# Kernel tuning notes

Hardware: AMD Instinct MI355X
Metric: run time of the kernel (lower is better)

The kernel has to match this reference:

```python
import jax, jax.numpy as jnp
import numpy as np

B, C, D, H, W, K = 2, 192, 48, 48, 48, 7
EPS_LN = 1e-6
EPS_GRN = 1e-6


def setup_inputs() -> dict:
    key = jax.random.key(0)
    ks = jax.random.split(key, 8)
    sc = 0.02
    return {
        "x": jax.random.normal(ks[0], (B, C, D, H, W), jnp.float32),
        # depthwise conv kernel in DHWIO layout: [K,K,K,1,C] (torch weight [C,1,K,K,K])
        "conv_w": jax.random.normal(ks[1], (K, K, K, 1, C), jnp.float32) * sc,
        "conv_b": jnp.zeros((C,), jnp.float32),
        "ln_g": jnp.ones((C,), jnp.float32),
        "ln_b": jnp.zeros((C,), jnp.float32),
        "w1": jax.random.normal(ks[2], (C, 4 * C), jnp.float32) * sc,
        "b1": jnp.zeros((4 * C,), jnp.float32),
        "grn_gamma": jax.random.normal(ks[3], (4 * C,), jnp.float32) * sc,
        "grn_beta": jax.random.normal(ks[4], (4 * C,), jnp.float32) * sc,
        "w2": jax.random.normal(ks[5], (4 * C, C), jnp.float32) * sc,
        "b2": jnp.zeros((C,), jnp.float32),
    }


def reference(x, conv_w, conv_b, ln_g, ln_b, w1, b1, grn_gamma, grn_beta, w2, b2):
    c = x.shape[1]
    # NCDHW -> NDHWC (channels-last, as Permute([0,2,3,4,1]) after the conv)
    xc = jnp.transpose(x, (0, 2, 3, 4, 1))
    # depthwise conv3d, kernel 7, pad 3 (SAME for stride 1)
    y = jax.lax.conv_general_dilated(
        xc, conv_w, window_strides=(1, 1, 1), padding="SAME",
        dimension_numbers=("NDHWC", "DHWIO", "NDHWC"),
        feature_group_count=c,
    ) + conv_b
    # LayerNorm over channel dim, eps=1e-6 (biased variance, like torch)
    mu = jnp.mean(y, axis=-1, keepdims=True)
    var = jnp.mean(jnp.square(y - mu), axis=-1, keepdims=True)
    y = (y - mu) * jax.lax.rsqrt(var + EPS_LN) * ln_g + ln_b
    # MLP up + exact GELU
    y = jax.nn.gelu(y @ w1 + b1, approximate=False)
    # GRN: global L2 over spatial dims per channel
    gx = jnp.sqrt(jnp.sum(y * y, axis=(1, 2, 3), keepdims=True))  # [B,1,1,1,4C]
    nx = gx / (jnp.mean(gx, axis=-1, keepdims=True) + EPS_GRN)
    y = grn_gamma * (y * nx) + grn_beta + y
    # MLP down, permute back, residual
    y = y @ w2 + b2
    return jnp.transpose(y, (0, 4, 1, 2, 3)) + x
```

## Files before the change

### kernel.cpp

```cpp
#include <hip/hip_runtime.h>
#include <math.h>

#define Bn 2
#define Cn 192
#define Dn 48
#define Hn 48
#define Wn 48
#define C4 768
#define DHW (Dn*Hn*Wn)
#define CDHW ((long)Cn*DHW)

typedef __attribute__((ext_vector_type(8))) short bf16x8;
typedef __attribute__((ext_vector_type(4))) float f32x4;

__device__ inline float bf2f(unsigned short u) {
    union { float f; unsigned int i; } v; v.i = ((unsigned int)u) << 16; return v.f;
}
__device__ inline unsigned short f2bf(float f) {
    union { float f; unsigned int i; } v; v.f = f;
    unsigned int r = v.i + 0x7FFFu + ((v.i >> 16) & 1u);
    return (unsigned short)(r >> 16);
}
__device__ inline float blo(unsigned int u) {
    union { unsigned int i; float f; } v; v.i = u << 16; return v.f;
}
__device__ inline float bhi(unsigned int u) {
    union { unsigned int i; float f; } v; v.i = u & 0xffff0000u; return v.f;
}
__device__ inline unsigned int cvtpk_bf16(float lo, float hi) {
    unsigned int r;
    asm("v_cvt_pk_bf16_f32 %0, %1, %2" : "=v"(r) : "v"(lo), "v"(hi));
    return r;
}
__device__ inline float gelu_tanh(float v) {
    float u = v * fmaf(0.0356774081f, v * v, 0.7978845608f);
    float a = fabsf(u);
    float t = __expf(-2.0f * a);
    float th = (1.0f - t) / (1.0f + t);
    th = copysignf(th, u);
    return 0.5f * v * (1.0f + th);
}

__global__ __launch_bounds__(256)
void xpad_k(const float* __restrict__ x, unsigned short* __restrict__ xbf)
{
    int u = blockIdx.x * 256 + threadIdx.x;
    int j = u & 7;
    int row = u >> 3;
    unsigned short* orow = xbf + ((size_t)row << 6);
    uint4 o = {0u, 0u, 0u, 0u};
    if (j >= 1 && j <= 6) {
        const float* xr = x + (size_t)row * 48 + (8 * j - 8);
        float4 a = *(const float4*)xr;
        float4 b = *(const float4*)(xr + 4);
        o.x = cvtpk_bf16(a.x, a.y); o.y = cvtpk_bf16(a.z, a.w);
        o.z = cvtpk_bf16(b.x, b.y); o.w = cvtpk_bf16(b.z, b.w);
    }
    *(uint4*)(orow + 8 * j) = o;
}

__global__ __launch_bounds__(256)
void btoep_k(const float* __restrict__ cw, unsigned short* __restrict__ btp)
{
    int idx = blockIdx.x * 256 + threadIdx.x;
    int lane = idx & 63;
    int t = idx >> 6;
    int kdkh = t % 49, c = t / 49;
    int n = lane & 15, g = lane >> 4;
    unsigned short v[8];
#pragma unroll
    for (int j = 0; j < 8; ++j) {
        int kw = 8 * g + j - n - 5;
        v[j] = (kw >= 0 && kw <= 6) ? f2bf(cw[(kdkh * 7 + kw) * Cn + c])
                                    : (unsigned short)0;
    }
    *(uint4*)(btp + (size_t)idx * 8) = *(uint4*)v;
}

#define CTD 16
#define CHD (CTD+6)
#define CHH 22

__global__ __launch_bounds__(128)
void conv_dw(const unsigned short* __restrict__ xbf, const unsigned short* __restrict__ btp,
             const float* __restrict__ cb, unsigned short* __restrict__ yc)
{
    __shared__ unsigned int xt[CHD * CHH * 16];
    int c = blockIdx.y;
    int s = blockIdx.x;
    int wt = s % 3, ht = (s / 3) % 3, dt = s / 9;
    int d0 = dt * 16, h0 = ht * 16, w0 = wt * 16;
    int tid = threadIdx.x;

    const unsigned short* xc = xbf + ((size_t)c * 2304 << 6);
    for (int u = tid; u < CHD * CHH * 4; u += 128) {
        int g = u & 3, r2 = u >> 2;
        int hh2 = r2 % CHH, dd = r2 / CHH;
        int gd = d0 - 3 + dd, gh = h0 - 3 + hh2;
        uint4 v = {0u, 0u, 0u, 0u};
        if ((unsigned)gd < 48u && (unsigned)gh < 48u)
            v = *(const uint4*)(xc + (((size_t)gd * 48 + gh) << 6) + w0 + 8 * g);
        *(uint4*)&xt[(r2 << 4) + ((g ^ (r2 & 3)) << 2)] = v;
    }
    __syncthreads();

    int lane = tid & 63, wv = tid >> 6;
    int lr = lane & 15, g = lane >> 4;
    float bias = cb[c];
    f32x4 acc[8];
#pragma unroll
    for (int t = 0; t < 8; ++t) acc[t] = (f32x4){bias, bias, bias, bias};

    const unsigned short* bchan = btp + (size_t)c * 49 * 512;
    const unsigned short* xt16 = (const unsigned short*)xt;

    for (int kh = 0; kh < 7; ++kh) {
        bf16x8 Bf[7];
#pragma unroll
        for (int kd = 0; kd < 7; ++kd)
            Bf[kd] = *(const bf16x8*)(bchan + (size_t)((kd * 7 + kh) * 64 + lane) * 8);
#pragma unroll
        for (int p = 0; p < 14; ++p) {
            int r2 = (8 * wv + p) * CHH + kh + lr;
            bf16x8 Af = *(const bf16x8*)(xt16 + (r2 << 5) + ((g ^ (r2 & 3)) << 3));
#pragma unroll
            for (int kd = 0; kd < 7; ++kd) {
                int t = p - kd;
                if (t < 0 || t > 7) continue;
                acc[t] = __builtin_amdgcn_mfma_f32_16x16x32_bf16(Af, Bf[kd], acc[t], 0, 0, 0);
            }
        }
    }

    unsigned short* yb = yc + (long)c * DHW;
#pragma unroll
    for (int t = 0; t < 8; ++t) {
        int d = d0 + 8 * wv + t;
#pragma unroll
        for (int i = 0; i < 4; ++i) {
            int h = h0 + g * 4 + i;
            yb[((long)d * 48 + h) * 48 + w0 + lr] = f2bf(acc[t][i]);
        }
    }
}

__global__ __launch_bounds__(256)
void ln_kernel(const unsigned short* __restrict__ yc, const float* __restrict__ g,
               const float* __restrict__ lb, unsigned short* __restrict__ y1)
{
    __shared__ float tile[Cn * Wn];
    __shared__ float qs1[4][48], qs2[4][48];
    __shared__ float mu_s[Wn], rs_s[Wn];
    int dh = blockIdx.x;
    long rowbase = (long)dh * Wn;
    for (int l = threadIdx.x; l < Cn * 24; l += 256) {
        int c = l / 24, wp = l % 24;
        unsigned int u = *(const unsigned int*)&yc[rowbase + (long)c * DHW + wp * 2];
        tile[c * Wn + wp * 2]     = blo(u);
        tile[c * Wn + wp * 2 + 1] = bhi(u);
    }
    __syncthreads();
    if (threadIdx.x < 192) {
        int w = threadIdx.x >> 2, q = threadIdx.x & 3;
        float s1 = 0.f, s2 = 0.f;
        for (int cc = 0; cc < 48; ++cc) {
            float v = tile[(cc * 4 + q) * Wn + w];
            s1 += v; s2 = fmaf(v, v, s2);
        }
        qs1[q][w] = s1; qs2[q][w] = s2;
    }
    __syncthreads();
    if (threadIdx.x < 48) {
        int w = threadIdx.x;
        float s1 = qs1[0][w] + qs1[1][w] + qs1[2][w] + qs1[3][w];
        float s2 = qs2[0][w] + qs2[1][w] + qs2[2][w] + qs2[3][w];
        float mu = s1 * (1.0f / Cn);
        float var = s2 * (1.0f / Cn) - mu * mu;
        mu_s[w] = mu;
        rs_s[w] = rsqrtf(var + 1e-6f);
    }
    __syncthreads();
    long obase = (long)dh * Wn * Cn;
    for (int l = threadIdx.x; l < Cn * Wn; l += 256) {
        int w = l / Cn, c = l % Cn;
        float val = (tile[c * Wn + w] - mu_s[w]) * rs_s[w] * g[c] + lb[c];
        y1[obase + l] = f2bf(val);
    }
}

__global__ __launch_bounds__(256)
void wtrans(const float* __restrict__ W, unsigned short* __restrict__ Wt, int K, int N)
{
    int idx = blockIdx.x * 256 + threadIdx.x;
    if (idx >= K * N) return;
    int n = idx / K, k = idx % K;
    Wt[idx] = f2bf(W[(long)k * N + n]);
}

__global__ __launch_bounds__(256)
void wscale(const float* __restrict__ W2, const float* __restrict__ gx2,
            const float* __restrict__ gamma, unsigned short* __restrict__ W2s)
{
    __shared__ float red[256];
    int t = threadIdx.x;
    float s = 0.f;
#pragma unroll
    for (int i = 0; i < 3; ++i) s += sqrtf(gx2[t + i * 256]);
    red[t] = s; __syncthreads();
    for (int st = 128; st > 0; st >>= 1) {
        if (t < st) red[t] += red[t + st];
        __syncthreads();
    }
    float inv = 1.0f / (red[0] * (1.0f / C4) + 1e-6f);
    int idx = blockIdx.x * 256 + t;
    int n = idx / C4, k = idx % C4;
    float snx = 1.0f + gamma[k] * sqrtf(gx2[k]) * inv;
    W2s[idx] = f2bf(W2[(long)k * Cn + n] * snx);
}

__global__ __launch_bounds__(256)
void gemm_up(const unsigned short* __restrict__ A, const unsigned short* __restrict__ Bt,
             const float* __restrict__ bias, unsigned short* __restrict__ Y2,
             float* __restrict__ partial)
{
    __shared__ short Asm[128 * Cn];
    __shared__ float colsum[2][C4];
    int tid = threadIdx.x;
    int lane = tid & 63, wv = tid >> 6;
    int wm = wv >> 1, wn = wv & 1;
    int lr = lane & 15, lq = lane >> 4;
    long m0 = (long)blockIdx.x * 128;

#pragma unroll
    for (int i = 0; i < 12; ++i) {
        int chunk = i * 256 + tid;
        int r = chunk / 24, cc = chunk - r * 24;
        bf16x8 v = *(const bf16x8*)(A + (size_t)(m0 + r) * Cn + cc * 8);
        *(bf16x8*)&Asm[r * Cn + ((cc ^ (r & 7)) * 8)] = v;
    }
    __syncthreads();

    for (int nt = 0; nt < 12; ++nt) {
        int n0 = nt * 64;
        f32x4 acc[4][2];
#pragma unroll
        for (int mi = 0; mi < 4; ++mi)
#pragma unroll
            for (int ni = 0; ni < 2; ++ni) acc[mi][ni] = (f32x4){0.f, 0.f, 0.f, 0.f};

#pragma unroll
        for (int ks = 0; ks < 6; ++ks) {
            bf16x8 af[4], bfr[2];
#pragma unroll
            for (int ni = 0; ni < 2; ++ni) {
                int nrow = n0 + wn * 32 + ni * 16 + lr;
                bfr[ni] = *(const bf16x8*)(Bt + (size_t)nrow * Cn + (ks * 4 + lq) * 8);
            }
#pragma unroll
            for (int mi = 0; mi < 4; ++mi) {
                int r = wm * 64 + mi * 16 + lr;
                int cc = (ks * 4 + lq) ^ (r & 7);
                af[mi] = *(const bf16x8*)&Asm[r * Cn + cc * 8];
            }
#pragma unroll
            for (int mi = 0; mi < 4; ++mi)
#pragma unroll
                for (int ni = 0; ni < 2; ++ni)
                    acc[mi][ni] = __builtin_amdgcn_mfma_f32_16x16x32_bf16(
                        af[mi], bfr[ni], acc[mi][ni], 0, 0, 0);
        }

        float ss[2] = {0.f, 0.f};
#pragma unroll
        for (int mi = 0; mi < 4; ++mi) {
#pragma unroll
            for (int ni = 0; ni < 2; ++ni) {
                int col = wn * 32 + ni * 16 + lr;
                float bb = bias[n0 + col];
                long row0 = m0 + wm * 64 + mi * 16 + lq * 4;
#pragma unroll
                for (int i = 0; i < 4; ++i) {
                    float v = gelu_tanh(acc[mi][ni][i] + bb);
                    ss[ni] = fmaf(v, v, ss[ni]);
                    Y2[(row0 + i) * C4 + n0 + col] = f2bf(v);
                }
            }
        }
#pragma unroll
        for (int ni = 0; ni < 2; ++ni) {
            ss[ni] += __shfl_xor(ss[ni], 16);
            ss[ni] += __shfl_xor(ss[ni], 32);
        }
        if (lq == 0) {
            colsum[wm][n0 + wn * 32 + lr]      = ss[0];
            colsum[wm][n0 + wn * 32 + 16 + lr] = ss[1];
        }
    }
    __syncthreads();
    for (int i = tid; i < C4; i += 256)
        partial[(size_t)blockIdx.x * C4 + i] = colsum[0][i] + colsum[1][i];
}

#define BM 128
#define BN 64
#define BK 64

#define GEMM_STAGE(Aptr, Astride, Btptr, Bstride)                               \
    {                                                                           \
        _Pragma("unroll")                                                       \
        for (int i = 0; i < 4; ++i) {                                           \
            int chunk = i * 256 + tid;                                          \
            int r = chunk >> 3, cc = chunk & 7;                                 \
            bf16x8 v = *(const bf16x8*)((Aptr) + (size_t)(m0 + r) * (Astride) + k0 + cc * 8); \
            *(bf16x8*)&Asm[r * BK + ((cc ^ (r & 7)) * 8)] = v;                  \
        }                                                                       \
        _Pragma("unroll")                                                       \
        for (int i = 0; i < 2; ++i) {                                           \
            int chunk = i * 256 + tid;                                          \
            int r = chunk >> 3, cc = chunk & 7;                                 \
            bf16x8 v = *(const bf16x8*)((Btptr) + (size_t)(n0 + r) * (Bstride) + k0 + cc * 8); \
            *(bf16x8*)&Bsm[r * BK + ((cc ^ (r & 7)) * 8)] = v;                  \
        }                                                                       \
    }

#define GEMM_COMPUTE                                                            \
    _Pragma("unroll")                                                           \
    for (int kk = 0; kk < 2; ++kk) {                                            \
        bf16x8 af[4], bfr[2];                                                   \
        _Pragma("unroll")                                                       \
        for (int mi = 0; mi < 4; ++mi) {                                        \
            int r = wm * 64 + mi * 16 + lr;                                     \
            int cc = (kk * 4 + lq) ^ (r & 7);                                   \
            af[mi] = *(const bf16x8*)&Asm[r * BK + cc * 8];                     \
        }                                                                       \
        _Pragma("unroll")                                                       \
        for (int ni = 0; ni < 2; ++ni) {                                        \
            int r = wn * 32 + ni * 16 + lr;                                     \
            int cc = (kk * 4 + lq) ^ (r & 7);                                   \
            bfr[ni] = *(const bf16x8*)&Bsm[r * BK + cc * 8];                    \
        }                                                                       \
        _Pragma("unroll")                                                       \
        for (int mi = 0; mi < 4; ++mi)                                          \
            _Pragma("unroll")                                                   \
            for (int ni = 0; ni < 2; ++ni)                                      \
                acc[mi][ni] = __builtin_amdgcn_mfma_f32_16x16x32_bf16(          \
                    af[mi], bfr[ni], acc[mi][ni], 0, 0, 0);                     \
    }

__global__ __launch_bounds__(256)
void gemm_down(const unsigned short* __restrict__ A, const unsigned short* __restrict__ Bt,
               const float* __restrict__ beff, const float* __restrict__ x,
               float* __restrict__ out)
{
    __shared__ short Asm[BM * BK];
    __shared__ short Bsm[BN * BK];
    int tid = threadIdx.x;
    int lane = tid & 63, wv = tid >> 6;
    int wm = wv >> 1, wn = wv & 1;
    int lr = lane & 15, lq = lane >> 4;
    long m0 = (long)blockIdx.y * BM;
    int n0 = blockIdx.x * BN;

    f32x4 acc[4][2];
#pragma unroll
    for (int mi = 0; mi < 4; ++mi)
#pragma unroll
        for (int ni = 0; ni < 2; ++ni) acc[mi][ni] = (f32x4){0.f, 0.f, 0.f, 0.f};

    for (int k0 = 0; k0 < C4; k0 += BK) {
        GEMM_STAGE(A, C4, Bt, C4);
        __syncthreads();
        GEMM_COMPUTE;
        __syncthreads();
    }

#pragma unroll
    for (int mi = 0; mi < 4; ++mi) {
#pragma unroll
        for (int ni = 0; ni < 2; ++ni) {
            int colg = n0 + wn * 32 + ni * 16 + lr;
            float be = beff[colg];
            long mbase = m0 + wm * 64 + mi * 16 + lq * 4;
            const float* xp = x + (long)colg * DHW + mbase;
            float* op = out + (long)colg * DHW + mbase;
            float4 xvv = *(const float4*)xp;
            float4 o;
            o.x = acc[mi][ni][0] + be + xvv.x;
            o.y = acc[mi][ni][1] + be + xvv.y;
            o.z = acc[mi][ni][2] + be + xvv.z;
            o.w = acc[mi][ni][3] + be + xvv.w;
            *(float4*)op = o;
        }
    }
}

__global__ __launch_bounds__(256)
void grn_reduce(const float* __restrict__ partial, float* __restrict__ gx2)
{
    int n = blockIdx.x;
    const float* p = partial + n;
    float s = 0.f;
    for (int r = threadIdx.x; r < 864; r += 256) s += p[(long)r * C4];
    __shared__ float red[256];
    red[threadIdx.x] = s; __syncthreads();
    for (int st = 128; st > 0; st >>= 1) {
        if (threadIdx.x < st) red[threadIdx.x] += red[threadIdx.x + st];
        __syncthreads();
    }
    if (threadIdx.x == 0) gx2[n] = red[0];
}

__global__ __launch_bounds__(256)
void bias_eff_k(const float* __restrict__ beta, const float* __restrict__ W2,
                const float* __restrict__ b2, float* __restrict__ beff)
{
    __shared__ float red[256];
    int j = blockIdx.x, t = threadIdx.x;
    float s = 0.f;
#pragma unroll
    for (int i = 0; i < 3; ++i) {
        int k = t + i * 256;
        s = fmaf(beta[k], W2[(long)k * Cn + j], s);
    }
    red[t] = s; __syncthreads();
    for (int st = 128; st > 0; st >>= 1) {
        if (t < st) red[t] += red[t + st];
        __syncthreads();
    }
    if (t == 0) beff[j] = red[0] + b2[j];
}

extern "C" void kernel_launch(void* const* d_in, const int* in_sizes, int n_in,
                              void* d_out, int out_size, void* d_ws, size_t ws_size,
                              hipStream_t stream) {
    const float* x      = (const float*)d_in[0];
    const float* conv_w = (const float*)d_in[1];
    const float* conv_b = (const float*)d_in[2];
    const float* ln_g   = (const float*)d_in[3];
    const float* ln_b   = (const float*)d_in[4];
    const float* w1     = (const float*)d_in[5];
    const float* b1     = (const float*)d_in[6];
    const float* gg     = (const float*)d_in[7];
    const float* gb     = (const float*)d_in[8];
    const float* w2     = (const float*)d_in[9];
    const float* b2     = (const float*)d_in[10];
    float* out = (float*)d_out;
    char* ws = (char*)d_ws;

    unsigned short* yc  = (unsigned short*)(ws);
    unsigned short* xbf = (unsigned short*)(ws + 42467328L);
    unsigned short* y2  = (unsigned short*)(ws);
    unsigned short* y1  = (unsigned short*)(ws + 169869312L);
    unsigned short* btp = (unsigned short*)(ws + 202702848L);
    float*     partial  = (float*)(ws + 212336640L);
    unsigned short* w1t = (unsigned short*)(ws + 214990848L);
    unsigned short* w2s = (unsigned short*)(ws + 215285760L);
    float*         gx2  = (float*)(ws + 215580672L);
    float*        beff  = (float*)(ws + 215586816L);

    bias_eff_k<<<Cn, 256, 0, stream>>>(gb, w2, b2, beff);
    wtrans<<<(Cn * C4 + 255) / 256, 256, 0, stream>>>(w1, w1t, Cn, C4);

    for (int b = 0; b < Bn; ++b) {
        const float* xb = x + (size_t)b * CDHW;
        float* outb = out + (size_t)b * CDHW;
        xpad_k<<<(Cn * 2304 * 8) / 256, 256, 0, stream>>>(xb, xbf);
        btoep_k<<<(Cn * 49 * 64) / 256, 256, 0, stream>>>(conv_w, btp);
        dim3 gc(27, Cn);
        conv_dw<<<gc, 128, 0, stream>>>(xbf, btp, conv_b, yc);
        ln_kernel<<<Dn * Hn, 256, 0, stream>>>(yc, ln_g, ln_b, y1);
        gemm_up<<<DHW / 128, 256, 0, stream>>>(y1, w1t, b1, y2, partial);
        grn_reduce<<<C4, 256, 0, stream>>>(partial, gx2);
        wscale<<<(Cn * C4) / 256, 256, 0, stream>>>(w2, gx2, gg, w2s);
        dim3 gd(Cn / BN, DHW / BM);
        gemm_down<<<gd, 256, 0, stream>>>(y2, w2s, beff, xb, outb);
    }
}
```

Measured before the change: 806.5 us.

## Compute all output channels per block in gemm_down, reading weights directly from global

gemm_down now has each block cover all 192 output channels (three 64-wide N tiles) for its 128-row M tile, so the large A activation tile is staged into LDS once instead of three times across separate blocks. The B (scaled weight) operand is no longer staged in LDS and is read straight from global memory through the cache for each MFMA fragment. This cuts global traffic for the bf16 intermediate, at the cost of triple the accumulator registers (lower occupancy), one third as many blocks, and uncoalesced global loads for the weight fragments.

```diff
diff --git a/kernel.cpp b/kernel.cpp
--- a/kernel.cpp
+++ b/kernel.cpp
@@ -301,95 +301,82 @@
         partial[(size_t)blockIdx.x * C4 + i] = colsum[0][i] + colsum[1][i];
 }
 
-#define BM 128
-#define BN 64
-#define BK 64
-
-#define GEMM_STAGE(Aptr, Astride, Btptr, Bstride)                               \
-    {                                                                           \
-        _Pragma("unroll")                                                       \
-        for (int i = 0; i < 4; ++i) {                                           \
-            int chunk = i * 256 + tid;                                          \
-            int r = chunk >> 3, cc = chunk & 7;                                 \
-            bf16x8 v = *(const bf16x8*)((Aptr) + (size_t)(m0 + r) * (Astride) + k0 + cc * 8); \
-            *(bf16x8*)&Asm[r * BK + ((cc ^ (r & 7)) * 8)] = v;                  \
-        }                                                                       \
-        _Pragma("unroll")                                                       \
-        for (int i = 0; i < 2; ++i) {                                           \
-            int chunk = i * 256 + tid;                                          \
-            int r = chunk >> 3, cc = chunk & 7;                                 \
-            bf16x8 v = *(const bf16x8*)((Btptr) + (size_t)(n0 + r) * (Bstride) + k0 + cc * 8); \
-            *(bf16x8*)&Bsm[r * BK + ((cc ^ (r & 7)) * 8)] = v;                  \
-        }                                                                       \
-    }
-
-#define GEMM_COMPUTE                                                            \
-    _Pragma("unroll")                                                           \
-    for (int kk = 0; kk < 2; ++kk) {                                            \
-        bf16x8 af[4], bfr[2];                                                   \
-        _Pragma("unroll")                                                       \
-        for (int mi = 0; mi < 4; ++mi) {                                        \
-            int r = wm * 64 + mi * 16 + lr;                                     \
-            int cc = (kk * 4 + lq) ^ (r & 7);                                   \
-            af[mi] = *(const bf16x8*)&Asm[r * BK + cc * 8];                     \
-        }                                                                       \
-        _Pragma("unroll")                                                       \
-        for (int ni = 0; ni < 2; ++ni) {                                        \
-            int r = wn * 32 + ni * 16 + lr;                                     \
-            int cc = (kk * 4 + lq) ^ (r & 7);                                   \
-            bfr[ni] = *(const bf16x8*)&Bsm[r * BK + cc * 8];                    \
-        }                                                                       \
-        _Pragma("unroll")                                                       \
-        for (int mi = 0; mi < 4; ++mi)                                          \
-            _Pragma("unroll")                                                   \
-            for (int ni = 0; ni < 2; ++ni)                                      \
-                acc[mi][ni] = __builtin_amdgcn_mfma_f32_16x16x32_bf16(          \
-                    af[mi], bfr[ni], acc[mi][ni], 0, 0, 0);                     \
-    }
-
 __global__ __launch_bounds__(256)
 void gemm_down(const unsigned short* __restrict__ A, const unsigned short* __restrict__ Bt,
                const float* __restrict__ beff, const float* __restrict__ x,
                float* __restrict__ out)
 {
-    __shared__ short Asm[BM * BK];
-    __shared__ short Bsm[BN * BK];
+    __shared__ short Asm[128 * 64];
     int tid = threadIdx.x;
     int lane = tid & 63, wv = tid >> 6;
     int wm = wv >> 1, wn = wv & 1;
     int lr = lane & 15, lq = lane >> 4;
-    long m0 = (long)blockIdx.y * BM;
-    int n0 = blockIdx.x * BN;
-
-    f32x4 acc[4][2];
-#pragma unroll
-    for (int mi = 0; mi < 4; ++mi)
-#pragma unroll
-        for (int ni = 0; ni < 2; ++ni) acc[mi][ni] = (f32x4){0.f, 0.f, 0.f, 0.f};
-
-    for (int k0 = 0; k0 < C4; k0 += BK) {
-        GEMM_STAGE(A, C4, Bt, C4);
+    long m0 = (long)blockIdx.x * 128;
+
+    f32x4 acc[3][4][2];
+#pragma unroll
+    for (int nt = 0; nt < 3; ++nt)
+#pragma unroll
+        for (int mi = 0; mi < 4; ++mi)
+#pragma unroll
+            for (int ni = 0; ni < 2; ++ni) acc[nt][mi][ni] = (f32x4){0.f, 0.f, 0.f, 0.f};
+
+    for (int k0 = 0; k0 < C4; k0 += 64) {
+#pragma unroll
+        for (int i = 0; i < 4; ++i) {
+            int chunk = i * 256 + tid;
+            int r = chunk >> 3, cc = chunk & 7;
+            bf16x8 v = *(const bf16x8*)(A + (size_t)(m0 + r) * C4 + k0 + cc * 8);
+            *(bf16x8*)&Asm[r * 64 + ((cc ^ (r & 7)) * 8)] = v;
+        }
         __syncthreads();
-        GEMM_COMPUTE;
+#pragma unroll
+        for (int ks = 0; ks < 2; ++ks) {
+            bf16x8 af[4];
+#pragma unroll
+            for (int mi = 0; mi < 4; ++mi) {
+                int r = wm * 64 + mi * 16 + lr;
+                int cc = (ks * 4 + lq) ^ (r & 7);
+                af[mi] = *(const bf16x8*)&Asm[r * 64 + cc * 8];
+            }
+#pragma unroll
+            for (int nt = 0; nt < 3; ++nt) {
+                bf16x8 bfr[2];
+#pragma unroll
+                for (int ni = 0; ni < 2; ++ni) {
+                    int nrow = nt * 64 + wn * 32 + ni * 16 + lr;
+                    bfr[ni] = *(const bf16x8*)(Bt + (size_t)nrow * C4 + k0 + (ks * 4 + lq) * 8);
+                }
+#pragma unroll
+                for (int mi = 0; mi < 4; ++mi)
+#pragma unroll
+                    for (int ni = 0; ni < 2; ++ni)
+                        acc[nt][mi][ni] = __builtin_amdgcn_mfma_f32_16x16x32_bf16(
+                            af[mi], bfr[ni], acc[nt][mi][ni], 0, 0, 0);
+            }
+        }
         __syncthreads();
     }
 
 #pragma unroll
-    for (int mi = 0; mi < 4; ++mi) {
-#pragma unroll
-        for (int ni = 0; ni < 2; ++ni) {
-            int colg = n0 + wn * 32 + ni * 16 + lr;
-            float be = beff[colg];
-            long mbase = m0 + wm * 64 + mi * 16 + lq * 4;
-            const float* xp = x + (long)colg * DHW + mbase;
-            float* op = out + (long)colg * DHW + mbase;
-            float4 xvv = *(const float4*)xp;
-            float4 o;
-            o.x = acc[mi][ni][0] + be + xvv.x;
-            o.y = acc[mi][ni][1] + be + xvv.y;
-            o.z = acc[mi][ni][2] + be + xvv.z;
-            o.w = acc[mi][ni][3] + be + xvv.w;
-            *(float4*)op = o;
+    for (int nt = 0; nt < 3; ++nt) {
+#pragma unroll
+        for (int mi = 0; mi < 4; ++mi) {
+#pragma unroll
+            for (int ni = 0; ni < 2; ++ni) {
+                int colg = nt * 64 + wn * 32 + ni * 16 + lr;
+                float be = beff[colg];
+                long mbase = m0 + wm * 64 + mi * 16 + lq * 4;
+                const float* xp = x + (long)colg * DHW + mbase;
+                float* op = out + (long)colg * DHW + mbase;
+                float4 xvv = *(const float4*)xp;
+                float4 o;
+                o.x = acc[nt][mi][ni][0] + be + xvv.x;
+                o.y = acc[nt][mi][ni][1] + be + xvv.y;
+                o.z = acc[nt][mi][ni][2] + be + xvv.z;
+                o.w = acc[nt][mi][ni][3] + be + xvv.w;
+                *(float4*)op = o;
+            }
         }
     }
 }
@@ -472,7 +459,6 @@
         gemm_up<<<DHW / 128, 256, 0, stream>>>(y1, w1t, b1, y2, partial);
         grn_reduce<<<C4, 256, 0, stream>>>(partial, gx2);
         wscale<<<(Cn * C4) / 256, 256, 0, stream>>>(w2, gx2, gg, w2s);
-        dim3 gd(Cn / BN, DHW / BM);
-        gemm_down<<<gd, 256, 0, stream>>>(y2, w2s, beff, xb, outb);
-    }
-}
+        gemm_down<<<DHW / 128, 256, 0, stream>>>(y2, w2s, beff, xb, outb);
+    }
+}
```

Result: slower. 858.6 us (+6.5%).
